# Kernel tuning notes

Hardware: AMD Instinct MI355X
Metric: run time of the kernel (lower is better)

Reference implementation:

```python
import jax, jax.numpy as jnp
import numpy as np

EPS_XVAR = 1e-06
EPS_QVAR = 1e-05
EPS_VAR = 1e-05
MIN_SCALE = 0.1  # rbf kernel
EPS_EDGE = 1e-06


def setup_inputs() -> dict:
    key = jax.random.key(0)
    k1, k2, k3, k4 = jax.random.split(key, 4)
    B, O, I, M = 2048, 64, 64, 32
    x = jax.random.normal(k1, (B, I), dtype=jnp.float32)
    # inducing locations: linspace(-1.5, 1.5, M) tiled over (O, I)
    z = jnp.broadcast_to(jnp.linspace(-1.5, 1.5, M, dtype=jnp.float32), (O, I, M))
    q_mu = jax.random.normal(k2, (O, I, M), dtype=jnp.float32) * 0.05
    q_log_var = jnp.full((O, I, M), -3.0, dtype=jnp.float32)
    log_scale = jnp.zeros((O, I), dtype=jnp.float32)
    log_variance = jnp.full((O, I), -1.0, dtype=jnp.float32)
    return {"x": x, "z": z, "q_mu": q_mu, "q_log_var": q_log_var,
            "log_scale": log_scale, "log_variance": log_variance}


def reference(x, z, q_mu, q_log_var, log_scale, log_variance):
    # x: [B, I]; params: [O, I, M] or [O, I]
    x_mean = x
    x_var = jnp.zeros_like(x) + EPS_XVAR

    q_var = jnp.maximum(jnp.exp(q_log_var), EPS_QVAR)           # [O, I, M]
    var_kern = jnp.maximum(jnp.exp(log_variance), EPS_VAR)      # [O, I]
    lengthscale = jnp.maximum(jnp.exp(log_scale), MIN_SCALE)    # [O, I]

    x_mu_exp = x_mean[:, None, :, None]        # [B, 1, I, 1]
    x_var_exp = x_var[:, None, :, None]        # [B, 1, I, 1]
    ell_sq = (lengthscale ** 2)[None, :, :, None]  # [1, O, I, 1]
    vk = var_kern[None, :, :, None]            # [1, O, I, 1]

    denom = ell_sq + x_var_exp                 # [B, O, I, 1]
    diff = x_mu_exp - z[None]                  # [B, O, I, M]
    psi_1 = vk * jnp.sqrt(ell_sq / denom) * jnp.exp(-0.5 * diff ** 2 / denom)

    edge_means = jnp.sum(psi_1 * q_mu[None], axis=-1)                      # [B, O, I]
    edge_vars = jnp.sum(psi_1 ** 2 * (q_var + q_mu ** 2)[None], axis=-1)   # [B, O, I]
    edge_vars = jnp.maximum(edge_vars - edge_means ** 2, EPS_EDGE)

    return edge_means.sum(axis=2), edge_vars.sum(axis=2)  # each [B, O]
```

## Files before the change

### kernel.cpp

```cpp
#include <hip/hip_runtime.h>

#define BATCH 2048
#define ODIM 64
#define IDIM 64
#define MDIM 32

static constexpr float LOG2E = 1.4426950408889634f;

#if __has_builtin(__builtin_amdgcn_exp2f)
#define EXP2F(x) __builtin_amdgcn_exp2f(x)
#else
#define EXP2F(x) exp2f(x)
#endif

typedef float v2f __attribute__((ext_vector_type(2)));

__global__ __launch_bounds__(512, 8) void gpkan_fused_kernel(
    const float* __restrict__ x, const float* __restrict__ z,
    const float* __restrict__ q_mu, const float* __restrict__ q_log_var,
    const float* __restrict__ log_scale, const float* __restrict__ log_variance,
    float* __restrict__ out)
{
    const int o     = blockIdx.x & (ODIM - 1);
    const int btile = blockIdx.x >> 6;
    const int tid   = threadIdx.x;
    const int lane  = tid & 63;
    const int wave  = __builtin_amdgcn_readfirstlane(tid >> 6);
    const int b0    = btile * 128 + 2 * lane;
    const int i0    = wave * 8;

    __shared__ float4 lds_c[IDIM][16];
    __shared__ float4 lds_aux[IDIM];
    __shared__ float  red[2][8][128];

    const float4* pA = (const float4*)(x + (size_t)b0 * IDIM + i0);
    const float4* pB = (const float4*)(x + (size_t)(b0 + 1) * IDIM + i0);
    float4 a0 = pA[0], a1 = pA[1];
    float4 bb0 = pB[0], bb1 = pB[1];

    #pragma unroll
    for (int rep = 0; rep < 2; ++rep) {
        const int q  = tid + rep * 512;
        const int i  = q >> 4;
        const int k  = q & 15;
        const int oi = o * IDIM + i;
        const int g  = oi * MDIM + 2 * k;

        const float ls = log_scale[oi];
        const float lv = log_variance[oi];
        const float ell   = fmaxf(expf(ls), 0.1f);
        const float ell2  = ell * ell;
        const float vk    = fmaxf(expf(lv), 1e-5f);
        const float denom = ell2 + 1e-6f;
        const float A = vk * sqrtf(ell2 / denom);
        const float a = -0.5f * LOG2E / denom;

        const float2 qm = *(const float2*)(q_mu + g);
        const float2 ql = *(const float2*)(q_log_var + g);
        const float2 zm = *(const float2*)(z + g);
        const float qv0 = fmaxf(expf(ql.x), 1e-5f);
        const float qv1 = fmaxf(expf(ql.y), 1e-5f);
        const float w0  = EXP2F(a * zm.x * zm.x);
        const float w1  = EXP2F(a * zm.y * zm.y);

        float4 c;
        c.x = A * qm.x * w0;
        c.y = A * A * (qv0 + qm.x * qm.x) * w0 * w0;
        c.z = A * qm.y * w1;
        c.w = A * A * (qv1 + qm.y * qm.y) * w1 * w1;
        lds_c[i][k] = c;

        if (k == 0)
            lds_aux[i] = make_float4(a, -2.0f * a * zm.x,
                                     -2.0f * a * (zm.y - zm.x), 0.0f);
    }
    __syncthreads();

    v2f xv[8];
    xv[0].x = a0.x; xv[0].y = bb0.x;
    xv[1].x = a0.y; xv[1].y = bb0.y;
    xv[2].x = a0.z; xv[2].y = bb0.z;
    xv[3].x = a0.w; xv[3].y = bb0.w;
    xv[4].x = a1.x; xv[4].y = bb1.x;
    xv[5].x = a1.y; xv[5].y = bb1.y;
    xv[6].x = a1.z; xv[6].y = bb1.z;
    xv[7].x = a1.w; xv[7].y = bb1.w;

    v2f emt = {0.f, 0.f};
    v2f evt = {0.f, 0.f};

    #pragma unroll
    for (int ii = 0; ii < 8; ++ii) {
        const float4 Ax = lds_aux[i0 + ii];
        const v2f x2 = xv[ii];

        v2f e1 = {Ax.x, Ax.x}, e2 = {Ax.y, Ax.y}, rc = {Ax.z, Ax.z};

        v2f t = __builtin_elementwise_fma(e1, x2, e2) * x2;
        v2f Eb;
        Eb.x = EXP2F(t.x); Eb.y = EXP2F(t.y);
        v2f ur = rc * x2;
        v2f rr;
        rr.x = EXP2F(ur.x); rr.y = EXP2F(ur.y);

        v2f s = rr * rr;
        v2f u = s * s;

        v2f Pe = {0.f, 0.f}, Po = {0.f, 0.f};
        v2f Qe = {0.f, 0.f}, Qo = {0.f, 0.f};

        const float4* C = &lds_c[i0 + ii][0];
        #pragma unroll
        for (int k = 15; k >= 0; --k) {
            float4 c = C[k];
            v2f c1e = {c.x, c.x}, c2e = {c.y, c.y};
            v2f c1o = {c.z, c.z}, c2o = {c.w, c.w};
            Pe = __builtin_elementwise_fma(Pe, s, c1e);
            Po = __builtin_elementwise_fma(Po, s, c1o);
            Qe = __builtin_elementwise_fma(Qe, u, c2e);
            Qo = __builtin_elementwise_fma(Qo, u, c2o);
        }

        v2f P = __builtin_elementwise_fma(rr, Po, Pe);
        v2f Q = __builtin_elementwise_fma(s,  Qo, Qe);

        v2f em_i = Eb * P;
        v2f ev_i = (Eb * Eb) * Q;

        v2f eps = {1e-6f, 1e-6f};
        v2f d   = __builtin_elementwise_fma(-em_i, em_i, ev_i);
        evt += __builtin_elementwise_max(d, eps);
        emt += em_i;
    }

    red[0][wave][2 * lane + 0] = emt.x;
    red[0][wave][2 * lane + 1] = emt.y;
    red[1][wave][2 * lane + 0] = evt.x;
    red[1][wave][2 * lane + 1] = evt.y;
    __syncthreads();

    if (tid < 256) {
        const int sel = tid >> 7;
        const int l   = tid & 127;
        float acc = 0.f;
        #pragma unroll
        for (int w = 0; w < 8; ++w) acc += red[sel][w][l];
        const int bb = btile * 128 + l;
        if (sel == 0) out[bb * ODIM + o] = acc;
        else          out[BATCH * ODIM + bb * ODIM + o] = acc;
    }
}

extern "C" void kernel_launch(void* const* d_in, const int* in_sizes, int n_in,
                              void* d_out, int out_size, void* d_ws, size_t ws_size,
                              hipStream_t stream) {
    const float* x            = (const float*)d_in[0];
    const float* z            = (const float*)d_in[1];
    const float* q_mu         = (const float*)d_in[2];
    const float* q_log_var    = (const float*)d_in[3];
    const float* log_scale    = (const float*)d_in[4];
    const float* log_variance = (const float*)d_in[5];
    float* out = (float*)d_out;

    (void)d_ws; (void)ws_size;

    gpkan_fused_kernel<<<dim3((BATCH / 128) * ODIM), dim3(512), 0, stream>>>(
        x, z, q_mu, q_log_var, log_scale, log_variance, out);
}
```

Baseline: 81.75 us.

## Map lanes to input dims, keep coefficients in registers, reduce with DPP

Each lane now owns one input dimension and keeps all 64 polynomial coefficients for it in registers, loaded once from a bank-swizzled LDS layout. Each wave then loops over 32 batch rows instead of re-reading coefficients from LDS per row. The cross-wave LDS reduction and barrier are replaced by per-wave LDS partial sums plus DPP row reductions that write outputs directly. Blocks cover 256 rows, so the grid is halved and launch bounds drop to 2 blocks. The risks are high register pressure, lower occupancy, and many small strided global stores.

New measurement: 84.46 us. +3.3%, slower.

```diff
diff --git a/kernel.cpp b/kernel.cpp
--- a/kernel.cpp
+++ b/kernel.cpp
@@ -4,6 +4,7 @@
 #define ODIM 64
 #define IDIM 64
 #define MDIM 32
+#define OUT_STRIDE (BATCH * ODIM)
 
 static constexpr float LOG2E = 1.4426950408889634f;
 
@@ -15,7 +16,14 @@
 
 typedef float v2f __attribute__((ext_vector_type(2)));
 
-__global__ __launch_bounds__(512, 8) void gpkan_fused_kernel(
+template <int CTRL>
+__device__ __forceinline__ float dpp_add(float v) {
+    int s = __builtin_amdgcn_update_dpp(0, __builtin_bit_cast(int, v),
+                                        CTRL, 0xF, 0xF, true);
+    return v + __builtin_bit_cast(float, s);
+}
+
+__global__ __launch_bounds__(512, 2) void gpkan_fused_kernel(
     const float* __restrict__ x, const float* __restrict__ z,
     const float* __restrict__ q_mu, const float* __restrict__ q_log_var,
     const float* __restrict__ log_scale, const float* __restrict__ log_variance,
@@ -25,18 +33,11 @@
     const int btile = blockIdx.x >> 6;
     const int tid   = threadIdx.x;
     const int lane  = tid & 63;
-    const int wave  = __builtin_amdgcn_readfirstlane(tid >> 6);
-    const int b0    = btile * 128 + 2 * lane;
-    const int i0    = wave * 8;
+    const int wave  = tid >> 6;
 
     __shared__ float4 lds_c[IDIM][16];
     __shared__ float4 lds_aux[IDIM];
-    __shared__ float  red[2][8][128];
-
-    const float4* pA = (const float4*)(x + (size_t)b0 * IDIM + i0);
-    const float4* pB = (const float4*)(x + (size_t)(b0 + 1) * IDIM + i0);
-    float4 a0 = pA[0], a1 = pA[1];
-    float4 bb0 = pB[0], bb1 = pB[1];
+    __shared__ __align__(16) float red[8][4][64];
 
     #pragma unroll
     for (int rep = 0; rep < 2; ++rep) {
@@ -68,86 +69,85 @@
         c.y = A * A * (qv0 + qm.x * qm.x) * w0 * w0;
         c.z = A * qm.y * w1;
         c.w = A * A * (qv1 + qm.y * qm.y) * w1 * w1;
-        lds_c[i][k] = c;
-
+        lds_c[i][(k + i) & 15] = c;
         if (k == 0)
             lds_aux[i] = make_float4(a, -2.0f * a * zm.x,
                                      -2.0f * a * (zm.y - zm.x), 0.0f);
     }
     __syncthreads();
 
-    v2f xv[8];
-    xv[0].x = a0.x; xv[0].y = bb0.x;
-    xv[1].x = a0.y; xv[1].y = bb0.y;
-    xv[2].x = a0.z; xv[2].y = bb0.z;
-    xv[3].x = a0.w; xv[3].y = bb0.w;
-    xv[4].x = a1.x; xv[4].y = bb1.x;
-    xv[5].x = a1.y; xv[5].y = bb1.y;
-    xv[6].x = a1.z; xv[6].y = bb1.z;
-    xv[7].x = a1.w; xv[7].y = bb1.w;
+    v2f C1e[16], C1o[16], C2e[16], C2o[16];
+    #pragma unroll
+    for (int k = 0; k < 16; ++k) {
+        const float4 q = lds_c[lane][(k + lane) & 15];
+        C1e[k] = (v2f){q.x, q.x};
+        C2e[k] = (v2f){q.y, q.y};
+        C1o[k] = (v2f){q.z, q.z};
+        C2o[k] = (v2f){q.w, q.w};
+    }
+    const float4 Ax = lds_aux[lane];
+    const v2f e1 = {Ax.x, Ax.x}, e2 = {Ax.y, Ax.y}, rc = {Ax.z, Ax.z};
 
-    v2f emt = {0.f, 0.f};
-    v2f evt = {0.f, 0.f};
+    const int bbase = btile * 256 + wave * 32;
+    float* redw = &red[wave][0][0];
+    const int v = lane >> 4, j = lane & 15;
 
     #pragma unroll
-    for (int ii = 0; ii < 8; ++ii) {
-        const float4 Ax = lds_aux[i0 + ii];
-        const v2f x2 = xv[ii];
+    for (int c = 0; c < 2; ++c) {
+        v2f xv[8];
+        #pragma unroll
+        for (int p = 0; p < 8; ++p) {
+            const int b0 = bbase + (c * 8 + p) * 2;
+            xv[p].x = x[(size_t)b0 * IDIM + lane];
+            xv[p].y = x[(size_t)(b0 + 1) * IDIM + lane];
+        }
+        #pragma unroll
+        for (int p = 0; p < 8; ++p) {
+            const int b0 = bbase + (c * 8 + p) * 2;
+            const v2f x2 = xv[p];
 
-        v2f e1 = {Ax.x, Ax.x}, e2 = {Ax.y, Ax.y}, rc = {Ax.z, Ax.z};
+            v2f t = __builtin_elementwise_fma(e1, x2, e2) * x2;
+            v2f Eb, rr;
+            Eb.x = EXP2F(t.x); Eb.y = EXP2F(t.y);
+            const v2f ur = rc * x2;
+            rr.x = EXP2F(ur.x); rr.y = EXP2F(ur.y);
+            const v2f s = rr * rr;
+            const v2f u = s * s;
 
-        v2f t = __builtin_elementwise_fma(e1, x2, e2) * x2;
-        v2f Eb;
-        Eb.x = EXP2F(t.x); Eb.y = EXP2F(t.y);
-        v2f ur = rc * x2;
-        v2f rr;
-        rr.x = EXP2F(ur.x); rr.y = EXP2F(ur.y);
+            v2f Pe = {0.f, 0.f}, Po = {0.f, 0.f};
+            v2f Qe = {0.f, 0.f}, Qo = {0.f, 0.f};
+            #pragma unroll
+            for (int k = 15; k >= 0; --k) {
+                Pe = __builtin_elementwise_fma(Pe, s, C1e[k]);
+                Po = __builtin_elementwise_fma(Po, s, C1o[k]);
+                Qe = __builtin_elementwise_fma(Qe, u, C2e[k]);
+                Qo = __builtin_elementwise_fma(Qo, u, C2o[k]);
+            }
+            const v2f P = __builtin_elementwise_fma(rr, Po, Pe);
+            const v2f Q = __builtin_elementwise_fma(s,  Qo, Qe);
 
-        v2f s = rr * rr;
-        v2f u = s * s;
+            const v2f em = Eb * P;
+            const v2f ev = (Eb * Eb) * Q;
+            const v2f eps = {1e-6f, 1e-6f};
+            const v2f d   = __builtin_elementwise_fma(-em, em, ev);
+            const v2f evc = __builtin_elementwise_max(d, eps);
 
-        v2f Pe = {0.f, 0.f}, Po = {0.f, 0.f};
-        v2f Qe = {0.f, 0.f}, Qo = {0.f, 0.f};
-
-        const float4* C = &lds_c[i0 + ii][0];
-        #pragma unroll
-        for (int k = 15; k >= 0; --k) {
-            float4 c = C[k];
-            v2f c1e = {c.x, c.x}, c2e = {c.y, c.y};
-            v2f c1o = {c.z, c.z}, c2o = {c.w, c.w};
-            Pe = __builtin_elementwise_fma(Pe, s, c1e);
-            Po = __builtin_elementwise_fma(Po, s, c1o);
-            Qe = __builtin_elementwise_fma(Qe, u, c2e);
-            Qo = __builtin_elementwise_fma(Qo, u, c2o);
+            redw[0 * 64 + lane] = em.x;
+            redw[1 * 64 + lane] = evc.x;
+            redw[2 * 64 + lane] = em.y;
+            redw[3 * 64 + lane] = evc.y;
+            asm volatile("s_waitcnt lgkmcnt(0)" ::: "memory");
+            const float4 qd = *(const float4*)&redw[v * 64 + j * 4];
+            float partial = (qd.x + qd.y) + (qd.z + qd.w);
+            partial = dpp_add<0xB1>(partial);
+            partial = dpp_add<0x4E>(partial);
+            partial = dpp_add<0x124>(partial);
+            partial = dpp_add<0x128>(partial);
+            if (j == 0) {
+                const int b = b0 + (v >> 1);
+                out[(size_t)(v & 1) * OUT_STRIDE + (size_t)b * ODIM + o] = partial;
+            }
         }
-
-        v2f P = __builtin_elementwise_fma(rr, Po, Pe);
-        v2f Q = __builtin_elementwise_fma(s,  Qo, Qe);
-
-        v2f em_i = Eb * P;
-        v2f ev_i = (Eb * Eb) * Q;
-
-        v2f eps = {1e-6f, 1e-6f};
-        v2f d   = __builtin_elementwise_fma(-em_i, em_i, ev_i);
-        evt += __builtin_elementwise_max(d, eps);
-        emt += em_i;
-    }
-
-    red[0][wave][2 * lane + 0] = emt.x;
-    red[0][wave][2 * lane + 1] = emt.y;
-    red[1][wave][2 * lane + 0] = evt.x;
-    red[1][wave][2 * lane + 1] = evt.y;
-    __syncthreads();
-
-    if (tid < 256) {
-        const int sel = tid >> 7;
-        const int l   = tid & 127;
-        float acc = 0.f;
-        #pragma unroll
-        for (int w = 0; w < 8; ++w) acc += red[sel][w][l];
-        const int bb = btile * 128 + l;
-        if (sel == 0) out[bb * ODIM + o] = acc;
-        else          out[BATCH * ODIM + bb * ODIM + o] = acc;
     }
 }
 
@@ -164,6 +164,6 @@
 
     (void)d_ws; (void)ws_size;
 
-    gpkan_fused_kernel<<<dim3((BATCH / 128) * ODIM), dim3(512), 0, stream>>>(
+    gpkan_fused_kernel<<<dim3((BATCH / 256) * ODIM), dim3(512), 0, stream>>>(
         x, z, q_mu, q_log_var, log_scale, log_variance, out);
 }
```
